# Kernel tuning notes

Hardware: AMD Instinct MI355X
Metric: run time of the kernel (lower is better)

## Reference

```python
import jax, jax.numpy as jnp
import numpy as np

BETA = 0.25  # qtz_beta


def setup_inputs() -> dict:
    key = jax.random.key(0)
    kz, kc = jax.random.split(key)
    N, D, K = 131072, 256, 1024
    z = jax.random.normal(kz, (N, D), dtype=jnp.float32)
    # torch init: uniform(-1/latent_dim, 1/latent_dim)
    codebook = jax.random.uniform(kc, (K, D), dtype=jnp.float32,
                                  minval=-1.0 / D, maxval=1.0 / D)
    return {"z": z, "codebook": codebook}


def reference(z, codebook):
    # pairwise squared distances: ||z||^2 - 2 z C^T + ||C||^2  -> [N, K]
    d = (jnp.sum(z * z, axis=-1, keepdims=True)
         - 2.0 * jnp.einsum('nd,kd->nk', z, codebook)
         + jnp.sum(codebook * codebook, axis=-1)[None, :])
    min_embed_ids = jnp.argmin(d, axis=-1)          # [N] int
    z_q = codebook[min_embed_ids]                   # gather == one_hot @ codebook
    # codebook loss (hard path, calculate_loss=True)
    codebook_loss = (jnp.mean((jax.lax.stop_gradient(z_q) - z) ** 2)
                     + BETA * jnp.mean((z_q - jax.lax.stop_gradient(z)) ** 2))
    # straight-through estimator
    z_q_st = z + jax.lax.stop_gradient(z_q - z)
    return (z, z_q_st, min_embed_ids, codebook_loss)
```

## Files before the change

kernel.cpp:

```cpp
#include <hip/hip_runtime.h>

#define N_TOK 131072
#define DIM   256
#define KCB   1024

#define RT    128
#define KT    128
#define TAU   1.0e-3f
#define EMIT_CAP 2048

typedef __attribute__((ext_vector_type(8))) short bf16x8;
typedef __attribute__((ext_vector_type(4))) float f32x4;

__device__ __forceinline__ unsigned short bf16_rtne(float v) {
  unsigned u = __float_as_uint(v);
  return (unsigned short)((u + 0x7FFFu + ((u >> 16) & 1u)) >> 16);
}
__device__ __forceinline__ float bf16_tof(unsigned short s) {
  return __uint_as_float(((unsigned)s) << 16);
}

__device__ __forceinline__ void gload_lds16(const short* g, short* l) {
  __builtin_amdgcn_global_load_lds(
      (const __attribute__((address_space(1))) void*)g,
      (__attribute__((address_space(3))) void*)l, 16, 0, 0);
}

__device__ __forceinline__ float np_sumsq_128(const float* __restrict__ p) {
#pragma clang fp contract(off)
  float4 a = *(const float4*)(p);
  float4 b = *(const float4*)(p + 4);
  float r0 = a.x * a.x, r1 = a.y * a.y, r2 = a.z * a.z, r3 = a.w * a.w;
  float r4 = b.x * b.x, r5 = b.y * b.y, r6 = b.z * b.z, r7 = b.w * b.w;
  for (int i = 8; i < 128; i += 8) {
    float4 c = *(const float4*)(p + i);
    float4 d = *(const float4*)(p + i + 4);
    r0 += c.x * c.x; r1 += c.y * c.y; r2 += c.z * c.z; r3 += c.w * c.w;
    r4 += d.x * d.x; r5 += d.y * d.y; r6 += d.z * d.z; r7 += d.w * d.w;
  }
  return ((r0 + r1) + (r2 + r3)) + ((r4 + r5) + (r6 + r7));
}

__global__ void prep_cc(const float* __restrict__ cb, float* __restrict__ cc,
                        double* __restrict__ loss_acc) {
  int k = blockIdx.x * blockDim.x + threadIdx.x;
  if (k == 0) *loss_acc = 0.0;
  if (k < KCB) {
    const float* p = cb + (long)k * DIM;
    cc[k] = np_sumsq_128(p) + np_sumsq_128(p + 128);
  }
}

__global__ void prep_split(const float* __restrict__ cb, short* __restrict__ ch,
                           short* __restrict__ cm) {
  int o = blockIdx.x * blockDim.x + threadIdx.x;
  if (o < KCB * DIM) {
    int dl = o & 7, k15 = (o >> 3) & 15, qd = (o >> 7) & 3;
    int ds = (o >> 9) & 7, kg = o >> 12;
    int k = kg * 16 + k15, d = ds * 32 + qd * 8 + dl;
    float v = cb[k * DIM + d];
    unsigned short h = bf16_rtne(v);
    ch[o] = (short)h;
    cm[o] = (short)bf16_rtne(v - bf16_tof(h));
  }
}

__global__ __launch_bounds__(256, 2)
void argmin_kernel(const float* __restrict__ z, const float* __restrict__ cb,
                   const short* __restrict__ ch_g, const short* __restrict__ cm_g,
                   const float* __restrict__ cc_g, float* __restrict__ ids_f) {
  __shared__ __align__(16) short cbuf[2][2][4096];
  __shared__ float zz_s[RT];
  __shared__ float zz_half[RT][2];
  __shared__ unsigned rowmin_s[RT];
  __shared__ int kmin_s[RT];
  __shared__ unsigned emit_s[EMIT_CAP];
  __shared__ int emit_cnt;

  const int t    = threadIdx.x;
  const int lane = t & 63;
  const int w    = t >> 6;
  const int l15  = lane & 15;
  const int qd   = lane >> 4;
  const long rowbase = (long)blockIdx.x * RT;

#pragma unroll
  for (int i = 0; i < 2; ++i) {
    int g = 2 * w + i;
    gload_lds16(ch_g + g * 4096 + lane * 8, (short*)&cbuf[0][0][0] + g * 512);
    gload_lds16(cm_g + g * 4096 + lane * 8, (short*)&cbuf[0][1][0] + g * 512);
  }

  {
    int r = t >> 1, h = t & 1;
    zz_half[r][h] = np_sumsq_128(z + (rowbase + r) * DIM + h * 128);
  }
  if (t < RT) { rowmin_s[t] = 0xFFFFFFFFu; kmin_s[t] = 0x7FFFFFFF; }
  if (t == 0) emit_cnt = 0;

  bf16x8 a_h[2][8], a_m[2][8];
  {
    const float* zp0 = z + (rowbase + 32 * w + l15) * (long)DIM + qd * 8;
#pragma unroll
    for (int m = 0; m < 2; ++m) {
      const float* zp = zp0 + m * 16 * DIM;
#pragma unroll
      for (int ds = 0; ds < 8; ++ds) {
        float4 v0 = *(const float4*)(zp + ds * 32);
        float4 v1 = *(const float4*)(zp + ds * 32 + 4);
        float f[8] = {v0.x, v0.y, v0.z, v0.w, v1.x, v1.y, v1.z, v1.w};
#pragma unroll
        for (int j = 0; j < 8; ++j) {
          unsigned short hh = bf16_rtne(f[j]);
          a_h[m][ds][j] = (short)hh;
          a_m[m][ds][j] = (short)bf16_rtne(f[j] - bf16_tof(hh));
        }
      }
    }
  }

  __syncthreads();
  if (t < RT) zz_s[t] = zz_half[t][0] + zz_half[t][1];

#pragma clang loop unroll(disable)
  for (int kt = 0; kt < 8; ++kt) {
    f32x4 acc[2][8];
#pragma unroll
    for (int m = 0; m < 2; ++m)
#pragma unroll
      for (int c = 0; c < 8; ++c) acc[m][c] = (f32x4){0.f, 0.f, 0.f, 0.f};

#pragma unroll
    for (int ds = 0; ds < 8; ++ds) {
      if (ds < 7 || kt < 7) {
        int ns = kt * 8 + ds + 1;
        long base = (long)(ns >> 3) * 32768 + (long)(ns & 7) * 512;
        short* dsth = (short*)&cbuf[(ds + 1) & 1][0][0];
        short* dstm = (short*)&cbuf[(ds + 1) & 1][1][0];
#pragma unroll
        for (int i = 0; i < 2; ++i) {
          int g = 2 * w + i;
          gload_lds16(ch_g + base + g * 4096 + lane * 8, dsth + g * 512);
          gload_lds16(cm_g + base + g * 4096 + lane * 8, dstm + g * 512);
        }
      }
      const short* bh = (const short*)&cbuf[ds & 1][0][0];
      const short* bm = (const short*)&cbuf[ds & 1][1][0];
#pragma unroll
      for (int c = 0; c < 8; ++c) {
        bf16x8 b_h = *(const bf16x8*)(bh + c * 512 + lane * 8);
        bf16x8 b_m = *(const bf16x8*)(bm + c * 512 + lane * 8);
#pragma unroll
        for (int m = 0; m < 2; ++m) {
          acc[m][c] = __builtin_amdgcn_mfma_f32_16x16x32_bf16(a_h[m][ds], b_h, acc[m][c], 0, 0, 0);
          acc[m][c] = __builtin_amdgcn_mfma_f32_16x16x32_bf16(a_h[m][ds], b_m, acc[m][c], 0, 0, 0);
          acc[m][c] = __builtin_amdgcn_mfma_f32_16x16x32_bf16(a_m[m][ds], b_h, acc[m][c], 0, 0, 0);
        }
      }
      if (ds < 7) __syncthreads();
    }

    float ccv[8];
#pragma unroll
    for (int c = 0; c < 8; ++c) ccv[c] = cc_g[kt * KT + 16 * c + l15];
    float rmin[2][4];
#pragma unroll
    for (int m = 0; m < 2; ++m)
#pragma unroll
      for (int rg = 0; rg < 4; ++rg) {
        int row = 32 * w + 16 * m + 4 * qd + rg;
        float zz = zz_s[row];
        float mn = __builtin_inff();
#pragma unroll
        for (int c = 0; c < 8; ++c) {
          float dv = (zz - 2.0f * acc[m][c][rg]) + ccv[c];
          mn = fminf(mn, dv);
        }
        rmin[m][rg] = mn;
      }
#pragma unroll
    for (int off = 1; off < 16; off <<= 1)
#pragma unroll
      for (int m = 0; m < 2; ++m)
#pragma unroll
        for (int rg = 0; rg < 4; ++rg)
          rmin[m][rg] = fminf(rmin[m][rg], __shfl_xor(rmin[m][rg], off, 64));
    if (l15 == 0) {
#pragma unroll
      for (int m = 0; m < 2; ++m)
#pragma unroll
        for (int rg = 0; rg < 4; ++rg)
          atomicMin(&rowmin_s[32 * w + 16 * m + 4 * qd + rg], __float_as_uint(rmin[m][rg]));
    }
    __syncthreads();
#pragma unroll
    for (int m = 0; m < 2; ++m)
#pragma unroll
      for (int rg = 0; rg < 4; ++rg) {
        int row = 32 * w + 16 * m + 4 * qd + rg;
        float th = __uint_as_float(rowmin_s[row]) + TAU;
        float zz = zz_s[row];
#pragma unroll
        for (int c = 0; c < 8; ++c) {
          int k = kt * KT + 16 * c + l15;
          float dv = (zz - 2.0f * acc[m][c][rg]) + ccv[c];
          if (dv <= th) {
            int idx = atomicAdd(&emit_cnt, 1);
            if (idx < EMIT_CAP) emit_s[idx] = ((unsigned)row << 10) | (unsigned)k;
          }
        }
      }
  }

  __syncthreads();
  int cnt = emit_cnt;
  bool over = cnt > EMIT_CAP;
  if (t < RT) rowmin_s[t] = 0xFFFFFFFFu;
  __syncthreads();

  if (!over) {
    unsigned mydd[8]; int myn[8], myk[8]; int mc = 0;
    for (int p = t; p < cnt; p += 256) {
      unsigned e = emit_s[p];
      int n = (int)(e >> 10), k = (int)(e & 1023);
      const float* zp = z + (rowbase + n) * DIM;
      const float* cp = cb + (long)k * DIM;
      float dot = 0.f;
      for (int d = 0; d < DIM; d += 4) {
        float4 zv = *(const float4*)(zp + d);
        float4 cv = *(const float4*)(cp + d);
        dot = fmaf(zv.x, cv.x, dot); dot = fmaf(zv.y, cv.y, dot);
        dot = fmaf(zv.z, cv.z, dot); dot = fmaf(zv.w, cv.w, dot);
      }
      float dd = (zz_s[n] - 2.0f * dot) + cc_g[k];
      mydd[mc] = __float_as_uint(dd); myn[mc] = n; myk[mc] = k; ++mc;
      atomicMin(&rowmin_s[n], __float_as_uint(dd));
    }
    __syncthreads();
    for (int i = 0; i < mc; ++i)
      if (mydd[i] == rowmin_s[myn[i]]) atomicMin(&kmin_s[myn[i]], myk[i]);
  } else {
    for (int p = t; p < RT * KCB; p += 256) {
      int n = p >> 10, k = p & 1023;
      const float* zp = z + (rowbase + n) * DIM;
      const float* cp = cb + (long)k * DIM;
      float dot = 0.f;
      for (int d = 0; d < DIM; d += 4) {
        float4 zv = *(const float4*)(zp + d);
        float4 cv = *(const float4*)(cp + d);
        dot = fmaf(zv.x, cv.x, dot); dot = fmaf(zv.y, cv.y, dot);
        dot = fmaf(zv.z, cv.z, dot); dot = fmaf(zv.w, cv.w, dot);
      }
      float dd = (zz_s[n] - 2.0f * dot) + cc_g[k];
      atomicMin(&rowmin_s[n], __float_as_uint(dd));
    }
    __syncthreads();
    for (int p = t; p < RT * KCB; p += 256) {
      int n = p >> 10, k = p & 1023;
      const float* zp = z + (rowbase + n) * DIM;
      const float* cp = cb + (long)k * DIM;
      float dot = 0.f;
      for (int d = 0; d < DIM; d += 4) {
        float4 zv = *(const float4*)(zp + d);
        float4 cv = *(const float4*)(cp + d);
        dot = fmaf(zv.x, cv.x, dot); dot = fmaf(zv.y, cv.y, dot);
        dot = fmaf(zv.z, cv.z, dot); dot = fmaf(zv.w, cv.w, dot);
      }
      float dd = (zz_s[n] - 2.0f * dot) + cc_g[k];
      if (__float_as_uint(dd) == rowmin_s[n]) atomicMin(&kmin_s[n], k);
    }
  }
  __syncthreads();
  if (t < RT) ids_f[rowbase + t] = (float)kmin_s[t];
}

__global__ void output_kernel(const float* __restrict__ z, const float* __restrict__ cb,
                              const float* __restrict__ ids_f,
                              float* __restrict__ out_z, float* __restrict__ out_zq,
                              double* __restrict__ loss_acc) {
  __shared__ double red[4];
  double acc = 0.0;
  const long total4 = (long)N_TOK * DIM / 4;
  long idx    = (long)blockIdx.x * blockDim.x + threadIdx.x;
  long stride = (long)gridDim.x * blockDim.x;
  for (long i = idx; i < total4; i += stride) {
    long e = i * 4;
    long r = e >> 8;
    int  k = (int)ids_f[r];
    float4 vz = *(const float4*)(z + e);
    float4 vc = *(const float4*)(cb + (long)k * DIM + (e & 255));
    *(float4*)(out_z + e)  = vz;
    *(float4*)(out_zq + e) = vc;
    float d0 = vc.x - vz.x, d1 = vc.y - vz.y, d2 = vc.z - vz.z, d3 = vc.w - vz.w;
    acc += (double)(d0 * d0) + (double)(d1 * d1) + (double)(d2 * d2) + (double)(d3 * d3);
  }
#pragma unroll
  for (int off = 32; off > 0; off >>= 1) acc += __shfl_down(acc, off, 64);
  int lane = threadIdx.x & 63, wv = threadIdx.x >> 6;
  if (lane == 0) red[wv] = acc;
  __syncthreads();
  if (threadIdx.x == 0) {
    double s = (red[0] + red[1]) + (red[2] + red[3]);
    atomicAdd(loss_acc, s);
  }
}

__global__ void finalize_kernel(const double* __restrict__ loss_acc,
                                float* __restrict__ out_loss) {
  if (threadIdx.x == 0) {
    double mean = *loss_acc / (double)((long)N_TOK * DIM);
    out_loss[0] = (float)(1.25 * mean);
  }
}

extern "C" void kernel_launch(void* const* d_in, const int* in_sizes, int n_in,
                              void* d_out, int out_size, void* d_ws, size_t ws_size,
                              hipStream_t stream) {
  const float* z  = (const float*)d_in[0];
  const float* cb = (const float*)d_in[1];
  float* out      = (float*)d_out;
  float* out_z    = out;
  float* out_zq   = out + (long)N_TOK * DIM;
  float* out_ids  = out_zq + (long)N_TOK * DIM;
  float* out_loss = out_ids + N_TOK;

  double* loss_acc = (double*)d_ws;

  short* ch_g = (short*)((char*)d_out);
  short* cm_g = (short*)((char*)d_out + 524288);
  float* cc_g = (float*)((char*)d_out + 1048576);

  prep_cc<<<4, 256, 0, stream>>>(cb, cc_g, loss_acc);
  prep_split<<<KCB * DIM / 256, 256, 0, stream>>>(cb, ch_g, cm_g);
  argmin_kernel<<<N_TOK / RT, 256, 0, stream>>>(z, cb, ch_g, cm_g, cc_g, out_ids);
  output_kernel<<<2048, 256, 0, stream>>>(z, cb, out_ids, out_z, out_zq, loss_acc);
  finalize_kernel<<<1, 64, 0, stream>>>(loss_acc, out_loss);
}
```

Before: 720.1 us.

## Replace split-bf16 triple MFMA with scaled single fp16 MFMA and wider rescoring band

Switches the distance GEMM from a three-pass hi/lo bf16 split to a single fp16 MFMA pass. The codebook is pre-scaled by 4096 so its small values fit fp16 range, and the accumulator is rescaled afterwards. The candidate threshold is widened and the emit buffer doubled so the exact fp32 rescoring pass can still recover the true argmin despite the lower precision. Dropping the low-part codebook halves LDS traffic and cuts MFMA work to a third. It also raises occupancy to 3 blocks per CU. The risks are more candidates to rescore, and an overflow fallback path when the emit buffer fills.

```diff
diff --git a/kernel.cpp b/kernel.cpp
--- a/kernel.cpp
+++ b/kernel.cpp
@@ -6,19 +6,13 @@
 
 #define RT    128
 #define KT    128
-#define TAU   1.0e-3f
-#define EMIT_CAP 2048
-
-typedef __attribute__((ext_vector_type(8))) short bf16x8;
+#define TAU   0.02f
+#define EMIT_CAP 4096
+#define CB_SCALE 4096.0f
+#define ACC_SCL  4.8828125e-4f
+
+typedef __attribute__((ext_vector_type(8))) _Float16 f16x8;
 typedef __attribute__((ext_vector_type(4))) float f32x4;
-
-__device__ __forceinline__ unsigned short bf16_rtne(float v) {
-  unsigned u = __float_as_uint(v);
-  return (unsigned short)((u + 0x7FFFu + ((u >> 16) & 1u)) >> 16);
-}
-__device__ __forceinline__ float bf16_tof(unsigned short s) {
-  return __uint_as_float(((unsigned)s) << 16);
-}
 
 __device__ __forceinline__ void gload_lds16(const short* g, short* l) {
   __builtin_amdgcn_global_load_lds(
@@ -51,25 +45,24 @@
   }
 }
 
-__global__ void prep_split(const float* __restrict__ cb, short* __restrict__ ch,
-                           short* __restrict__ cm) {
+__global__ void prep_h16(const float* __restrict__ cb, short* __restrict__ ch) {
   int o = blockIdx.x * blockDim.x + threadIdx.x;
   if (o < KCB * DIM) {
     int dl = o & 7, k15 = (o >> 3) & 15, qd = (o >> 7) & 3;
-    int ds = (o >> 9) & 7, kg = o >> 12;
-    int k = kg * 16 + k15, d = ds * 32 + qd * 8 + dl;
-    float v = cb[k * DIM + d];
-    unsigned short h = bf16_rtne(v);
-    ch[o] = (short)h;
-    cm[o] = (short)bf16_rtne(v - bf16_tof(h));
-  }
-}
-
-__global__ __launch_bounds__(256, 2)
+    int dsl = (o >> 9) & 1, kg8 = (o >> 10) & 7;
+    int p = (o >> 13) & 3, kt = (o >> 15) & 7;
+    int k = kt * 128 + kg8 * 16 + k15;
+    int d = (2 * p + dsl) * 32 + qd * 8 + dl;
+    float v = cb[k * DIM + d] * CB_SCALE;
+    ((_Float16*)ch)[o] = (_Float16)v;
+  }
+}
+
+__global__ __launch_bounds__(256, 3)
 void argmin_kernel(const float* __restrict__ z, const float* __restrict__ cb,
-                   const short* __restrict__ ch_g, const short* __restrict__ cm_g,
+                   const short* __restrict__ ch_g,
                    const float* __restrict__ cc_g, float* __restrict__ ids_f) {
-  __shared__ __align__(16) short cbuf[2][2][4096];
+  __shared__ __align__(16) short cbuf[2][8192];
   __shared__ float zz_s[RT];
   __shared__ float zz_half[RT][2];
   __shared__ unsigned rowmin_s[RT];
@@ -85,10 +78,9 @@
   const long rowbase = (long)blockIdx.x * RT;
 
 #pragma unroll
-  for (int i = 0; i < 2; ++i) {
-    int g = 2 * w + i;
-    gload_lds16(ch_g + g * 4096 + lane * 8, (short*)&cbuf[0][0][0] + g * 512);
-    gload_lds16(cm_g + g * 4096 + lane * 8, (short*)&cbuf[0][1][0] + g * 512);
+  for (int j = 0; j < 4; ++j) {
+    int off = w * 2048 + j * 512 + lane * 8;
+    gload_lds16(ch_g + off, &cbuf[0][0] + off);
   }
 
   {
@@ -98,7 +90,7 @@
   if (t < RT) { rowmin_s[t] = 0xFFFFFFFFu; kmin_s[t] = 0x7FFFFFFF; }
   if (t == 0) emit_cnt = 0;
 
-  bf16x8 a_h[2][8], a_m[2][8];
+  f16x8 a16[2][8];
   {
     const float* zp0 = z + (rowbase + 32 * w + l15) * (long)DIM + qd * 8;
 #pragma unroll
@@ -110,11 +102,7 @@
         float4 v1 = *(const float4*)(zp + ds * 32 + 4);
         float f[8] = {v0.x, v0.y, v0.z, v0.w, v1.x, v1.y, v1.z, v1.w};
 #pragma unroll
-        for (int j = 0; j < 8; ++j) {
-          unsigned short hh = bf16_rtne(f[j]);
-          a_h[m][ds][j] = (short)hh;
-          a_m[m][ds][j] = (short)bf16_rtne(f[j] - bf16_tof(hh));
-        }
+        for (int j = 0; j < 8; ++j) a16[m][ds][j] = (_Float16)f[j];
       }
     }
   }
@@ -131,33 +119,26 @@
       for (int c = 0; c < 8; ++c) acc[m][c] = (f32x4){0.f, 0.f, 0.f, 0.f};
 
 #pragma unroll
-    for (int ds = 0; ds < 8; ++ds) {
-      if (ds < 7 || kt < 7) {
-        int ns = kt * 8 + ds + 1;
-        long base = (long)(ns >> 3) * 32768 + (long)(ns & 7) * 512;
-        short* dsth = (short*)&cbuf[(ds + 1) & 1][0][0];
-        short* dstm = (short*)&cbuf[(ds + 1) & 1][1][0];
-#pragma unroll
-        for (int i = 0; i < 2; ++i) {
-          int g = 2 * w + i;
-          gload_lds16(ch_g + base + g * 4096 + lane * 8, dsth + g * 512);
-          gload_lds16(cm_g + base + g * 4096 + lane * 8, dstm + g * 512);
+    for (int p = 0; p < 4; ++p) {
+      int s = kt * 4 + p;
+      if (s < 31) {
+        const short* src = ch_g + (long)(s + 1) * 8192;
+#pragma unroll
+        for (int j = 0; j < 4; ++j) {
+          int off = w * 2048 + j * 512 + lane * 8;
+          gload_lds16(src + off, &cbuf[(p + 1) & 1][0] + off);
         }
       }
-      const short* bh = (const short*)&cbuf[ds & 1][0][0];
-      const short* bm = (const short*)&cbuf[ds & 1][1][0];
-#pragma unroll
-      for (int c = 0; c < 8; ++c) {
-        bf16x8 b_h = *(const bf16x8*)(bh + c * 512 + lane * 8);
-        bf16x8 b_m = *(const bf16x8*)(bm + c * 512 + lane * 8);
-#pragma unroll
-        for (int m = 0; m < 2; ++m) {
-          acc[m][c] = __builtin_amdgcn_mfma_f32_16x16x32_bf16(a_h[m][ds], b_h, acc[m][c], 0, 0, 0);
-          acc[m][c] = __builtin_amdgcn_mfma_f32_16x16x32_bf16(a_h[m][ds], b_m, acc[m][c], 0, 0, 0);
-          acc[m][c] = __builtin_amdgcn_mfma_f32_16x16x32_bf16(a_m[m][ds], b_h, acc[m][c], 0, 0, 0);
+#pragma unroll
+      for (int dsl = 0; dsl < 2; ++dsl) {
+#pragma unroll
+        for (int c = 0; c < 8; ++c) {
+          f16x8 b = *(const f16x8*)&cbuf[p & 1][c * 1024 + dsl * 512 + lane * 8];
+          acc[0][c] = __builtin_amdgcn_mfma_f32_16x16x32_f16(a16[0][2 * p + dsl], b, acc[0][c], 0, 0, 0);
+          acc[1][c] = __builtin_amdgcn_mfma_f32_16x16x32_f16(a16[1][2 * p + dsl], b, acc[1][c], 0, 0, 0);
         }
       }
-      if (ds < 7) __syncthreads();
+      if (p < 3) __syncthreads();
     }
 
     float ccv[8];
@@ -173,7 +154,7 @@
         float mn = __builtin_inff();
 #pragma unroll
         for (int c = 0; c < 8; ++c) {
-          float dv = (zz - 2.0f * acc[m][c][rg]) + ccv[c];
+          float dv = (zz - acc[m][c][rg] * ACC_SCL) + ccv[c];
           mn = fminf(mn, dv);
         }
         rmin[m][rg] = mn;
@@ -203,7 +184,7 @@
 #pragma unroll
         for (int c = 0; c < 8; ++c) {
           int k = kt * KT + 16 * c + l15;
-          float dv = (zz - 2.0f * acc[m][c][rg]) + ccv[c];
+          float dv = (zz - acc[m][c][rg] * ACC_SCL) + ccv[c];
           if (dv <= th) {
             int idx = atomicAdd(&emit_cnt, 1);
             if (idx < EMIT_CAP) emit_s[idx] = ((unsigned)row << 10) | (unsigned)k;
@@ -219,7 +200,7 @@
   __syncthreads();
 
   if (!over) {
-    unsigned mydd[8]; int myn[8], myk[8]; int mc = 0;
+    unsigned mydd[16]; int myn[16], myk[16]; int mc = 0;
     for (int p = t; p < cnt; p += 256) {
       unsigned e = emit_s[p];
       int n = (int)(e >> 10), k = (int)(e & 1023);
@@ -327,12 +308,11 @@
   double* loss_acc = (double*)d_ws;
 
   short* ch_g = (short*)((char*)d_out);
-  short* cm_g = (short*)((char*)d_out + 524288);
-  float* cc_g = (float*)((char*)d_out + 1048576);
+  float* cc_g = (float*)((char*)d_out + 524288);
 
   prep_cc<<<4, 256, 0, stream>>>(cb, cc_g, loss_acc);
-  prep_split<<<KCB * DIM / 256, 256, 0, stream>>>(cb, ch_g, cm_g);
-  argmin_kernel<<<N_TOK / RT, 256, 0, stream>>>(z, cb, ch_g, cm_g, cc_g, out_ids);
+  prep_h16<<<KCB * DIM / 256, 256, 0, stream>>>(cb, ch_g);
+  argmin_kernel<<<N_TOK / RT, 256, 0, stream>>>(z, cb, ch_g, cc_g, out_ids);
   output_kernel<<<2048, 256, 0, stream>>>(z, cb, out_ids, out_z, out_zq, loss_acc);
   finalize_kernel<<<1, 64, 0, stream>>>(loss_acc, out_loss);
 }
```

Result: slower. 770.7 us (+7.0%).
